# Kernel tuning notes

Hardware: AMD Instinct MI355X
Metric: run time of the kernel (lower is better)

Reference implementation:

```python
import jax, jax.numpy as jnp
import numpy as np

N_NODES = 50000
N_EDGES = 1600000
NUM_REL = 3
HID = 64
IN_DIM = 3
EDGE_DIM = 6
DEC_H = 32
Q1, Q2 = 5000.0, 10000.0


def _glorot(key, shape):
    fan_in, fan_out = shape[-2], shape[-1]
    lim = float(np.sqrt(6.0 / (fan_in + fan_out)))
    return jax.random.uniform(key, shape, jnp.float32, -lim, lim)


def setup_inputs() -> dict:
    key = jax.random.key(0)
    ks = jax.random.split(key, 20)
    x = jax.random.normal(ks[0], (N_NODES, IN_DIM), jnp.float32)
    edge_index = jax.random.randint(ks[1], (2, N_EDGES), 0, N_NODES, jnp.int64)
    edge_attr = jax.random.uniform(ks[2], (N_EDGES, EDGE_DIM), jnp.float32)
    # first column is distance in km; spread over [0, 15000) to hit all 3 bins
    edge_attr = edge_attr.at[:, 0].set(edge_attr[:, 0] * 15000.0)
    inp = {"x": x, "edge_index": edge_index, "edge_attr": edge_attr}
    dims = [IN_DIM, HID, HID]
    for i, din in enumerate(dims):
        inp[f"w{i}"] = _glorot(ks[3 + 3 * i], (NUM_REL, din, HID))
        inp[f"root{i}"] = _glorot(ks[4 + 3 * i], (din, HID))
        inp[f"b{i}"] = jnp.zeros((HID,), jnp.float32)
    dec_in = 2 * HID + EDGE_DIM
    inp["dw1"] = _glorot(ks[13], (dec_in, DEC_H))
    inp["db1"] = jnp.zeros((DEC_H,), jnp.float32)
    inp["dw2"] = _glorot(ks[14], (DEC_H, DEC_H // 2))
    inp["db2"] = jnp.zeros((DEC_H // 2,), jnp.float32)
    inp["dw3"] = _glorot(ks[15], (DEC_H // 2, 1))
    inp["db3"] = jnp.zeros((1,), jnp.float32)
    return inp


def _rgcn_conv(x, src, dst, edge_type, W, root, b):
    # PyG RGCNConv: per-relation mean aggregation of neighbor features,
    # then transform; plus root weight and bias.
    n = x.shape[0]
    xj = x[src]  # [E, in] gather
    out = x @ root + b
    for r in range(NUM_REL):
        m = (edge_type == r).astype(x.dtype)[:, None]  # [E,1]
        s = jax.ops.segment_sum(xj * m, dst, num_segments=n)   # [N,in]
        c = jax.ops.segment_sum(m, dst, num_segments=n)        # [N,1]
        h = s / jnp.maximum(c, 1.0)
        out = out + h @ W[r]
    return out


def reference(x, edge_index, edge_attr,
              w0, root0, b0, w1, root1, b1, w2, root2, b2,
              dw1, db1, dw2, db2, dw3, db3):
    dist = edge_attr[:, 0]
    edge_type = (dist > Q1).astype(jnp.int32) + (dist > Q2).astype(jnp.int32)
    src, dst = edge_index[0], edge_index[1]
    h = x
    for W, root, b in ((w0, root0, b0), (w1, root1, b1), (w2, root2, b2)):
        h = jax.nn.relu(_rgcn_conv(h, src, dst, edge_type, W, root, b))
        # dropout is identity in eval mode
    dec_in = jnp.concatenate([h[src], h[dst], edge_attr], axis=-1)  # [E, 134]
    z = jax.nn.relu(dec_in @ dw1 + db1)
    z = jax.nn.relu(z @ dw2 + db2)
    return (z @ dw3 + db3).squeeze(-1)
```

## Files before the change

kernel.cpp:

```cpp
#include <hip/hip_runtime.h>
#include <stdint.h>

#define N_NODES 50000
#define N_EDGES 1600000
#define NBLK_N 196
#define NB 391
#define BPAD 8192
#define CHUNK 4096
#define NWG_PREP 391

__device__ inline float bf2f(uint16_t u) {
  union { uint32_t i; float f; } c; c.i = (uint32_t)u << 16; return c.f;
}
__device__ inline uint16_t f2bf(float f) {
  union { uint32_t i; float f; } c; c.f = f;
  uint32_t b = c.i;
  b += 0x7FFFu + ((b >> 16) & 1u);
  return (uint16_t)(b >> 16);
}

__device__ inline uint32_t enc8(float v) {
  union { float f; uint32_t i; } c; c.f = v;
  uint32_t u = c.i;
  int t = (int)(((u + 0x80000u) >> 20) & 0x7FFu) - 960;
  t = t < 0 ? 0 : (t > 126 ? 126 : t);
  return ((u >> 24) & 0x80u) | (uint32_t)t;
}
__device__ inline float dec8(uint32_t b) {
  uint32_t m = b & 0x7Fu;
  union { uint32_t i; float f; } c;
  c.i = ((b & 0x80u) << 24) | ((m + 960u) << 20);
  return m ? c.f : 0.0f;
}

__global__ __launch_bounds__(256) void k_prep(const int* __restrict__ ei,
                                              const float* __restrict__ ea,
                                              int* __restrict__ bcur,
                                              uint32_t* __restrict__ pairbuf) {
  __shared__ int hist[NB];
  __shared__ int hbase[NB];
  int t = threadIdx.x;
  int base = blockIdx.x * CHUNK;
  for (int i = t; i < NB; i += 256) hist[i] = 0;
  __syncthreads();

  uint32_t wreg[16];
  int breg[16];
  #pragma unroll
  for (int k = 0; k < 16; k++) {
    int e = base + t + k * 256;
    breg[k] = -1;
    if (e < N_EDGES) {
      float dist = ea[(size_t)e * 6];
      int rel = (dist > 5000.0f) + (dist > 10000.0f);
      int s = ei[e];
      int d = ei[N_EDGES + e];
      wreg[k] = (uint32_t)s | ((uint32_t)rel << 16) | ((uint32_t)(d & 127) << 24);
      breg[k] = d >> 7;
      atomicAdd(&hist[breg[k]], 1);
    }
  }
  __syncthreads();
  for (int i = t; i < NB; i += 256) {
    int h = hist[i];
    hbase[i] = h ? atomicAdd(&bcur[i], h) : 0;
    hist[i] = 0;
  }
  __syncthreads();
  #pragma unroll
  for (int k = 0; k < 16; k++) {
    int b = breg[k];
    if (b >= 0) {
      int r = atomicAdd(&hist[b], 1);
      pairbuf[(size_t)b * BPAD + hbase[b] + r] = wreg[k];
    }
  }
}

__global__ __launch_bounds__(256) void k_count(const uint32_t* __restrict__ pairbuf,
                                               const int* __restrict__ bcur,
                                               int* __restrict__ cnt3) {
  __shared__ int lc[384];
  int b = blockIdx.x;
  int t = threadIdx.x;
  for (int i = t; i < 384; i += 256) lc[i] = 0;
  int cnt = bcur[b];
  __syncthreads();
  const uint32_t* pb = pairbuf + (size_t)b * BPAD;
  for (int i = t; i < cnt; i += 256) {
    uint32_t w = pb[i];
    int dl  = (int)(w >> 24);
    int rel = (int)((w >> 16) & 3u);
    atomicAdd(&lc[dl * 3 + rel], 1);
  }
  __syncthreads();
  int gbase = b * 384;
  for (int j = t; j < 384; j += 256) {
    int node = (b << 7) + (j / 3);
    if (node < N_NODES) cnt3[gbase + j] = lc[j];
  }
}

__global__ __launch_bounds__(256) void k_scanA(const int* __restrict__ cnt3,
                                               int* __restrict__ excl,
                                               int* __restrict__ bsum) {
  __shared__ int s[256];
  int t = threadIdx.x;
  int n = blockIdx.x * 256 + t;
  int deg = 0;
  if (n < N_NODES) deg = cnt3[3 * n] + cnt3[3 * n + 1] + cnt3[3 * n + 2];
  s[t] = deg;
  __syncthreads();
  for (int ofs = 1; ofs < 256; ofs <<= 1) {
    int v = (t >= ofs) ? s[t - ofs] : 0;
    __syncthreads();
    s[t] += v;
    __syncthreads();
  }
  if (n < N_NODES) excl[n] = s[t] - deg;
  if (t == 255) bsum[blockIdx.x] = s[255];
}

__global__ __launch_bounds__(256) void k_scanB(int* __restrict__ bsum) {
  __shared__ int s[256];
  int t = threadIdx.x;
  int v = (t < NBLK_N) ? bsum[t] : 0;
  s[t] = v;
  __syncthreads();
  for (int ofs = 1; ofs < 256; ofs <<= 1) {
    int u = (t >= ofs) ? s[t - ofs] : 0;
    __syncthreads();
    s[t] += u;
    __syncthreads();
  }
  if (t < NBLK_N) bsum[t] = s[t] - v;
}

__global__ __launch_bounds__(256) void k_scanC(const int* __restrict__ cnt3,
                                               const int* __restrict__ excl,
                                               const int* __restrict__ bsum,
                                               int4* __restrict__ meta,
                                               const float* __restrict__ x,
                                               float4* __restrict__ x4) {
  int n = blockIdx.x * 256 + threadIdx.x;
  if (n >= N_NODES) return;
  meta[n] = make_int4(bsum[blockIdx.x] + excl[n],
                      cnt3[3 * n], cnt3[3 * n + 1], cnt3[3 * n + 2]);
  x4[n] = make_float4(x[n * 3], x[n * 3 + 1], x[n * 3 + 2], 0.0f);
}

__global__ __launch_bounds__(256) void k_scat2(const uint32_t* __restrict__ pairbuf,
                                               const int* __restrict__ bcur,
                                               const int4* __restrict__ meta,
                                               uint32_t* __restrict__ csr) {
  __shared__ int lcur[128];
  int b = blockIdx.x;
  int t = threadIdx.x;
  int node0 = b << 7;
  if (t < 128) {
    int n = node0 + t;
    lcur[t] = (n < N_NODES) ? meta[n].x : 0;
  }
  int cnt = bcur[b];
  __syncthreads();
  const uint32_t* pb = pairbuf + (size_t)b * BPAD;
  for (int i = t; i < cnt; i += 256) {
    uint32_t w = pb[i];
    int dl = (int)(w >> 24);
    int p = atomicAdd(&lcur[dl], 1);
    csr[p] = w & 0x00FFFFFFu;
  }
}

__global__ __launch_bounds__(256) void k_layer0(const float4* __restrict__ x4,
                                                const float* __restrict__ W0,
                                                const float* __restrict__ root0,
                                                const float* __restrict__ b0,
                                                const int4* __restrict__ meta,
                                                const uint32_t* __restrict__ csr,
                                                float* __restrict__ hout,
                                                uint16_t* __restrict__ hbf) {
  __shared__ float sW[576], sR[192], sb[64];
  int t = threadIdx.x;
  for (int i = t; i < 576; i += 256) sW[i] = W0[i];
  for (int i = t; i < 192; i += 256) sR[i] = root0[i];
  if (t < 64) sb[t] = b0[t];
  __syncthreads();
  int wid = t >> 6, lane = t & 63;
  int n = blockIdx.x * 4 + wid;
  int4 md = meta[n];
  int off = md.x, c0 = md.y, c1 = md.z, c2 = md.w;
  int cnt = c0 + c1 + c2;
  float a00 = 0, a01 = 0, a02 = 0, a10 = 0, a11 = 0, a12 = 0, a20 = 0, a21 = 0, a22 = 0;
  for (int base = 0; base < cnt; base += 64) {
    int idx = base + lane;
    float4 v = make_float4(0, 0, 0, 0);
    int r = 3;
    if (idx < cnt) {
      uint32_t u = csr[off + idx];
      r = (int)(u >> 16);
      v = x4[u & 0xFFFFu];
    }
    a00 += (r == 0) ? v.x : 0.0f; a01 += (r == 0) ? v.y : 0.0f; a02 += (r == 0) ? v.z : 0.0f;
    a10 += (r == 1) ? v.x : 0.0f; a11 += (r == 1) ? v.y : 0.0f; a12 += (r == 1) ? v.z : 0.0f;
    a20 += (r == 2) ? v.x : 0.0f; a21 += (r == 2) ? v.y : 0.0f; a22 += (r == 2) ? v.z : 0.0f;
  }
  #pragma unroll
  for (int d = 1; d < 64; d <<= 1) {
    a00 += __shfl_xor(a00, d); a01 += __shfl_xor(a01, d); a02 += __shfl_xor(a02, d);
    a10 += __shfl_xor(a10, d); a11 += __shfl_xor(a11, d); a12 += __shfl_xor(a12, d);
    a20 += __shfl_xor(a20, d); a21 += __shfl_xor(a21, d); a22 += __shfl_xor(a22, d);
  }
  float i0 = 1.0f / (float)(c0 > 1 ? c0 : 1);
  float i1 = 1.0f / (float)(c1 > 1 ? c1 : 1);
  float i2 = 1.0f / (float)(c2 > 1 ? c2 : 1);
  float4 xn = x4[n];
  float in[12];
  in[0] = xn.x; in[1] = xn.y; in[2] = xn.z;
  in[3] = a00 * i0; in[4] = a01 * i0; in[5] = a02 * i0;
  in[6] = a10 * i1; in[7] = a11 * i1; in[8] = a12 * i1;
  in[9] = a20 * i2; in[10] = a21 * i2; in[11] = a22 * i2;
  float acc = sb[lane];
  #pragma unroll
  for (int k = 0; k < 3; k++) acc = fmaf(in[k], sR[k * 64 + lane], acc);
  #pragma unroll
  for (int k = 0; k < 9; k++) acc = fmaf(in[3 + k], sW[k * 64 + lane], acc);
  float h = fmaxf(acc, 0.0f);
  hout[(size_t)n * 64 + lane] = h;
  hbf[(size_t)n * 64 + lane] = f2bf(h);
}

#define ACC(E, V) { int r_ = (int)((E) >> 16); \
  a0 += (r_ == 0) ? (V) : 0.0f; a1 += (r_ == 1) ? (V) : 0.0f; a2 += (r_ == 2) ? (V) : 0.0f; }

__global__ __launch_bounds__(256) void k_agg(const uint16_t* __restrict__ hbf,
                                             const int4* __restrict__ meta,
                                             const uint32_t* __restrict__ csr,
                                             float* __restrict__ mbuf) {
  int t = threadIdx.x, wid = t >> 6, lane = t & 63;
  int n = blockIdx.x * 4 + wid;
  int4 md = meta[n];
  int off = __builtin_amdgcn_readfirstlane(md.x);
  int c0  = __builtin_amdgcn_readfirstlane(md.y);
  int c1  = __builtin_amdgcn_readfirstlane(md.z);
  int c2  = __builtin_amdgcn_readfirstlane(md.w);
  int cnt = c0 + c1 + c2;
  const uint32_t* cp = csr + off;
  float a0 = 0, a1 = 0, a2 = 0;
  int i = 0;
  for (; i + 8 <= cnt; i += 8) {
    uint32_t e0 = cp[i],     e1 = cp[i + 1], e2 = cp[i + 2], e3 = cp[i + 3];
    uint32_t e4 = cp[i + 4], e5 = cp[i + 5], e6 = cp[i + 6], e7 = cp[i + 7];
    float v0 = bf2f(hbf[(int)((e0 & 0xFFFFu) << 6) + lane]);
    float v1 = bf2f(hbf[(int)((e1 & 0xFFFFu) << 6) + lane]);
    float v2 = bf2f(hbf[(int)((e2 & 0xFFFFu) << 6) + lane]);
    float v3 = bf2f(hbf[(int)((e3 & 0xFFFFu) << 6) + lane]);
    float v4 = bf2f(hbf[(int)((e4 & 0xFFFFu) << 6) + lane]);
    float v5 = bf2f(hbf[(int)((e5 & 0xFFFFu) << 6) + lane]);
    float v6 = bf2f(hbf[(int)((e6 & 0xFFFFu) << 6) + lane]);
    float v7 = bf2f(hbf[(int)((e7 & 0xFFFFu) << 6) + lane]);
    ACC(e0, v0) ACC(e1, v1) ACC(e2, v2) ACC(e3, v3)
    ACC(e4, v4) ACC(e5, v5) ACC(e6, v6) ACC(e7, v7)
  }
  for (; i < cnt; i++) {
    uint32_t e = cp[i];
    float v = bf2f(hbf[(int)((e & 0xFFFFu) << 6) + lane]);
    ACC(e, v)
  }
  float* mb = mbuf + (size_t)n * 192;
  mb[lane]       = a0 * (1.0f / (float)(c0 > 1 ? c0 : 1));
  mb[64 + lane]  = a1 * (1.0f / (float)(c1 > 1 ? c1 : 1));
  mb[128 + lane] = a2 * (1.0f / (float)(c2 > 1 ? c2 : 1));
}

__global__ __launch_bounds__(256) void k_gemm(const float* __restrict__ hin,
                                              const float* __restrict__ mbuf,
                                              const float* __restrict__ W,
                                              const float* __restrict__ root,
                                              const float* __restrict__ b,
                                              float* __restrict__ hout,
                                              uint16_t* __restrict__ hbf) {
  __shared__ float As[64 * 84];
  __shared__ float Bs[64 * 64];
  __shared__ float sb[64];
  int t = threadIdx.x;
  int bn = blockIdx.x * 64;
  if (t < 64) sb[t] = b[t];
  int tn = t & 15, to = t >> 4;
  float acc[4][4] = {};
  for (int kb = 0; kb < 4; kb++) {
    const float4* Bsrc = (const float4*)((kb == 0) ? root : (W + (size_t)(kb - 1) * 4096));
    for (int i2 = t; i2 < 1024; i2 += 256) ((float4*)Bs)[i2] = Bsrc[i2];
    int r = t >> 2;
    int node = bn + r;
    bool ok = node < N_NODES;
    const float* Arow = (kb == 0) ? (hin + (size_t)node * 64)
                                  : (mbuf + (size_t)node * 192 + (size_t)(kb - 1) * 64);
    #pragma unroll
    for (int ii = 0; ii < 4; ii++) {
      int c4 = (t & 3) + 4 * ii;
      float4 v = ok ? ((const float4*)Arow)[c4] : make_float4(0, 0, 0, 0);
      *(float4*)&As[r * 84 + c4 * 4] = v;
    }
    __syncthreads();
    #pragma unroll
    for (int k4 = 0; k4 < 16; k4++) {
      float4 a0 = *(const float4*)&As[(tn)      * 84 + k4 * 4];
      float4 a1 = *(const float4*)&As[(tn + 16) * 84 + k4 * 4];
      float4 a2 = *(const float4*)&As[(tn + 32) * 84 + k4 * 4];
      float4 a3 = *(const float4*)&As[(tn + 48) * 84 + k4 * 4];
      float4 b0 = *(const float4*)&Bs[(k4 * 4 + 0) * 64 + to * 4];
      float4 b1 = *(const float4*)&Bs[(k4 * 4 + 1) * 64 + to * 4];
      float4 b2 = *(const float4*)&Bs[(k4 * 4 + 2) * 64 + to * 4];
      float4 b3 = *(const float4*)&Bs[(k4 * 4 + 3) * 64 + to * 4];
      const float* av[4] = {&a0.x, &a1.x, &a2.x, &a3.x};
      const float* bv[4] = {&b0.x, &b1.x, &b2.x, &b3.x};
      #pragma unroll
      for (int c = 0; c < 4; c++)
        #pragma unroll
        for (int i3 = 0; i3 < 4; i3++)
          #pragma unroll
          for (int j = 0; j < 4; j++)
            acc[i3][j] = fmaf(av[i3][c], bv[c][j], acc[i3][j]);
    }
    __syncthreads();
  }
  #pragma unroll
  for (int i3 = 0; i3 < 4; i3++) {
    int node = bn + tn + 16 * i3;
    if (node < N_NODES) {
      float4 o;
      o.x = fmaxf(acc[i3][0] + sb[to * 4 + 0], 0.0f);
      o.y = fmaxf(acc[i3][1] + sb[to * 4 + 1], 0.0f);
      o.z = fmaxf(acc[i3][2] + sb[to * 4 + 2], 0.0f);
      o.w = fmaxf(acc[i3][3] + sb[to * 4 + 3], 0.0f);
      *(float4*)(hout + (size_t)node * 64 + to * 4) = o;
      if (hbf) {
        uint2 pk;
        pk.x = (uint32_t)f2bf(o.x) | ((uint32_t)f2bf(o.y) << 16);
        pk.y = (uint32_t)f2bf(o.z) | ((uint32_t)f2bf(o.w) << 16);
        *(uint2*)(hbf + (size_t)node * 64 + to * 4) = pk;
      }
    }
  }
}

__global__ __launch_bounds__(256) void k_pq2(const float* __restrict__ h,
                                             const float* __restrict__ dw1,
                                             const float* __restrict__ db1,
                                             uint8_t* __restrict__ Pb,
                                             uint8_t* __restrict__ Qb) {
  __shared__ float As[64 * 84];
  __shared__ float Bs[64 * 64];
  __shared__ float sdb1[32];
  int t = threadIdx.x;
  int bn = blockIdx.x * 64;
  if (t < 32) sdb1[t] = db1[t];
  {
    int r = t >> 2;
    int node = bn + r;
    bool ok = node < N_NODES;
    const float* Arow = h + (size_t)node * 64;
    #pragma unroll
    for (int ii = 0; ii < 4; ii++) {
      int c4 = (t & 3) + 4 * ii;
      float4 v = ok ? ((const float4*)Arow)[c4] : make_float4(0, 0, 0, 0);
      *(float4*)&As[r * 84 + c4 * 4] = v;
    }
  }
  for (int i = t; i < 4096; i += 256) {
    int k = i >> 6, j = i & 63;
    Bs[i] = (j < 32) ? dw1[k * 32 + j] : dw1[(64 + k) * 32 + (j - 32)];
  }
  __syncthreads();
  int tn = t & 15, to = t >> 4;
  float acc[4][4] = {};
  #pragma unroll
  for (int k4 = 0; k4 < 16; k4++) {
    float4 a0 = *(const float4*)&As[(tn)      * 84 + k4 * 4];
    float4 a1 = *(const float4*)&As[(tn + 16) * 84 + k4 * 4];
    float4 a2 = *(const float4*)&As[(tn + 32) * 84 + k4 * 4];
    float4 a3 = *(const float4*)&As[(tn + 48) * 84 + k4 * 4];
    float4 b0 = *(const float4*)&Bs[(k4 * 4 + 0) * 64 + to * 4];
    float4 b1 = *(const float4*)&Bs[(k4 * 4 + 1) * 64 + to * 4];
    float4 b2 = *(const float4*)&Bs[(k4 * 4 + 2) * 64 + to * 4];
    float4 b3 = *(const float4*)&Bs[(k4 * 4 + 3) * 64 + to * 4];
    const float* av[4] = {&a0.x, &a1.x, &a2.x, &a3.x};
    const float* bv[4] = {&b0.x, &b1.x, &b2.x, &b3.x};
    #pragma unroll
    for (int c = 0; c < 4; c++)
      #pragma unroll
      for (int i3 = 0; i3 < 4; i3++)
        #pragma unroll
        for (int j = 0; j < 4; j++)
          acc[i3][j] = fmaf(av[i3][c], bv[c][j], acc[i3][j]);
  }
  bool isP = (to < 8);
  float bias0 = isP ? sdb1[to * 4 + 0] : 0.0f;
  float bias1 = isP ? sdb1[to * 4 + 1] : 0.0f;
  float bias2 = isP ? sdb1[to * 4 + 2] : 0.0f;
  float bias3 = isP ? sdb1[to * 4 + 3] : 0.0f;
  #pragma unroll
  for (int i3 = 0; i3 < 4; i3++) {
    int node = bn + tn + 16 * i3;
    if (node < N_NODES) {
      uint32_t pk = enc8(acc[i3][0] + bias0)
                  | (enc8(acc[i3][1] + bias1) << 8)
                  | (enc8(acc[i3][2] + bias2) << 16)
                  | (enc8(acc[i3][3] + bias3) << 24);
      if (isP) *(uint32_t*)(Pb + (size_t)node * 32 + to * 4) = pk;
      else     *(uint32_t*)(Qb + (size_t)node * 32 + (to - 8) * 4) = pk;
    }
  }
}

__global__ __launch_bounds__(256) void k_dec(const int* __restrict__ ei,
                                             const float* __restrict__ ea,
                                             const uint8_t* __restrict__ Pb,
                                             const uint8_t* __restrict__ Qb,
                                             const float* __restrict__ dw1,
                                             const float* __restrict__ dw2,
                                             const float* __restrict__ db2,
                                             const float* __restrict__ dw3,
                                             const float* __restrict__ db3,
                                             float* __restrict__ out) {
  __shared__ float C[6 * 32], W2[32 * 16], sb2[16], W3[16];
  __shared__ float sb3;
  int t = threadIdx.x;
  for (int i = t; i < 192; i += 256) C[i] = dw1[128 * 32 + i];
  for (int i = t; i < 512; i += 256) W2[i] = dw2[i];
  if (t < 16) { sb2[t] = db2[t]; W3[t] = dw3[t]; }
  if (t == 0) sb3 = db3[0];
  __syncthreads();
  int e = blockIdx.x * 256 + t;
  int s = ei[e];
  int d = ei[N_EDGES + e];
  float ea6[6];
  #pragma unroll
  for (int i = 0; i < 6; i++) ea6[i] = ea[(size_t)e * 6 + i];
  uint4 pv0 = *(const uint4*)(Pb + (size_t)s * 32);
  uint4 pv1 = *(const uint4*)(Pb + (size_t)s * 32 + 16);
  uint4 qv0 = *(const uint4*)(Qb + (size_t)d * 32);
  uint4 qv1 = *(const uint4*)(Qb + (size_t)d * 32 + 16);
  uint32_t pw[8] = {pv0.x, pv0.y, pv0.z, pv0.w, pv1.x, pv1.y, pv1.z, pv1.w};
  uint32_t qw[8] = {qv0.x, qv0.y, qv0.z, qv0.w, qv1.x, qv1.y, qv1.z, qv1.w};
  float z1[32];
  #pragma unroll
  for (int w = 0; w < 8; w++) {
    #pragma unroll
    for (int c = 0; c < 4; c++) {
      int j = w * 4 + c;
      float v = dec8((pw[w] >> (8 * c)) & 0xFFu) + dec8((qw[w] >> (8 * c)) & 0xFFu);
      #pragma unroll
      for (int k = 0; k < 6; k++) v = fmaf(ea6[k], C[k * 32 + j], v);
      z1[j] = fmaxf(v, 0.0f);
    }
  }
  float o = sb3;
  #pragma unroll
  for (int i = 0; i < 16; i++) {
    float z = sb2[i];
    #pragma unroll
    for (int j = 0; j < 32; j++) z = fmaf(z1[j], W2[j * 16 + i], z);
    o = fmaf(fmaxf(z, 0.0f), W3[i], o);
  }
  out[e] = o;
}

extern "C" void kernel_launch(void* const* d_in, const int* in_sizes, int n_in,
                              void* d_out, int out_size, void* d_ws, size_t ws_size,
                              hipStream_t stream) {
  const float* x      = (const float*)d_in[0];
  const int*   ei     = (const int*)d_in[1];
  const float* ea     = (const float*)d_in[2];
  const float* w0     = (const float*)d_in[3];
  const float* root0  = (const float*)d_in[4];
  const float* b0     = (const float*)d_in[5];
  const float* w1     = (const float*)d_in[6];
  const float* root1  = (const float*)d_in[7];
  const float* b1     = (const float*)d_in[8];
  const float* w2     = (const float*)d_in[9];
  const float* root2  = (const float*)d_in[10];
  const float* b2     = (const float*)d_in[11];
  const float* dw1    = (const float*)d_in[12];
  const float* db1    = (const float*)d_in[13];
  const float* dw2    = (const float*)d_in[14];
  const float* db2    = (const float*)d_in[15];
  const float* dw3    = (const float*)d_in[16];
  const float* db3    = (const float*)d_in[17];
  float* out = (float*)d_out;

  char* w = (char*)d_ws;
  int* cnt3        = (int*)w;       w += (size_t)N_NODES * 3 * 4;
  int* bcur        = (int*)w;       w += (size_t)NB * 4;
  int4* meta       = (int4*)w;      w += (size_t)N_NODES * 16;
  uint32_t* csr    = (uint32_t*)w;  w += (size_t)N_EDGES * 4;
  float4* x4       = (float4*)w;    w += (size_t)N_NODES * 16;
  float* h1        = (float*)w;     w += (size_t)N_NODES * 64 * 4;
  float* h2        = (float*)w;     w += (size_t)N_NODES * 64 * 4;
  float* mbuf      = (float*)w;     w += (size_t)N_NODES * 192 * 4;
  uint16_t* hbf1   = (uint16_t*)w;  w += (size_t)N_NODES * 64 * 2;
  uint16_t* hbf2   = (uint16_t*)w;  w += (size_t)N_NODES * 64 * 2;
  uint8_t* Pb      = (uint8_t*)hbf1;
  uint8_t* Qb      = (uint8_t*)hbf2;
  uint32_t* pairbuf = (uint32_t*)h1;
  int* excl        = (int*)mbuf;
  int* bsum        = (int*)mbuf + N_NODES;

  hipMemsetAsync(bcur, 0, (size_t)NB * 4, stream);

  k_prep   <<<NWG_PREP, 256, 0, stream>>>(ei, ea, bcur, pairbuf);
  k_count  <<<NB, 256, 0, stream>>>(pairbuf, bcur, cnt3);
  k_scanA  <<<NBLK_N, 256, 0, stream>>>(cnt3, excl, bsum);
  k_scanB  <<<1, 256, 0, stream>>>(bsum);
  k_scanC  <<<NBLK_N, 256, 0, stream>>>(cnt3, excl, bsum, meta, x, x4);
  k_scat2  <<<NB, 256, 0, stream>>>(pairbuf, bcur, meta, csr);

  k_layer0 <<<N_NODES / 4, 256, 0, stream>>>(x4, w0, root0, b0, meta, csr, h1, hbf1);

  k_agg    <<<N_NODES / 4, 256, 0, stream>>>(hbf1, meta, csr, mbuf);
  k_gemm   <<<(N_NODES + 63) / 64, 256, 0, stream>>>(h1, mbuf, w1, root1, b1, h2, hbf2);

  k_agg    <<<N_NODES / 4, 256, 0, stream>>>(hbf2, meta, csr, mbuf);
  k_gemm   <<<(N_NODES + 63) / 64, 256, 0, stream>>>(h2, mbuf, w2, root2, b2, h1, (uint16_t*)nullptr);

  k_pq2    <<<(N_NODES + 63) / 64, 256, 0, stream>>>(h1, dw1, db1, Pb, Qb);
  k_dec    <<<N_EDGES / 256, 256, 0, stream>>>(ei, ea, Pb, Qb, dw1, dw2, db2, dw3, db3, out);
}
```

Before: 350.5 us.

## Store gathered node features in hardware FP8 and vectorize decoder weight reads

Hidden features gathered by the aggregation kernels are now stored as 8-bit FP8 instead of bf16, halving the bytes pulled per neighbour gather. The custom software 8-bit encode and decode in the P/Q and decoder path is replaced by hardware FP8 pack and convert instructions. The decoder also transposes W2 in shared memory so it can be read with float4 loads. FP8 E4M3 keeps fewer mantissa bits than bf16, so the mean aggregation loses precision, and values are clamped at 440.

```diff
diff --git a/kernel.cpp b/kernel.cpp
--- a/kernel.cpp
+++ b/kernel.cpp
@@ -9,28 +9,20 @@
 #define CHUNK 4096
 #define NWG_PREP 391
 
+typedef float fvec2 __attribute__((ext_vector_type(2)));
+
 __device__ inline float bf2f(uint16_t u) {
   union { uint32_t i; float f; } c; c.i = (uint32_t)u << 16; return c.f;
 }
-__device__ inline uint16_t f2bf(float f) {
-  union { uint32_t i; float f; } c; c.f = f;
-  uint32_t b = c.i;
-  b += 0x7FFFu + ((b >> 16) & 1u);
-  return (uint16_t)(b >> 16);
-}
-
-__device__ inline uint32_t enc8(float v) {
-  union { float f; uint32_t i; } c; c.f = v;
-  uint32_t u = c.i;
-  int t = (int)(((u + 0x80000u) >> 20) & 0x7FFu) - 960;
-  t = t < 0 ? 0 : (t > 126 ? 126 : t);
-  return ((u >> 24) & 0x80u) | (uint32_t)t;
-}
-__device__ inline float dec8(uint32_t b) {
-  uint32_t m = b & 0x7Fu;
-  union { uint32_t i; float f; } c;
-  c.i = ((b & 0x80u) << 24) | ((m + 960u) << 20);
-  return m ? c.f : 0.0f;
+
+__device__ inline uint32_t pk4_fp8(float a, float b, float c, float d) {
+  a = fminf(fmaxf(a, -440.0f), 440.0f);
+  b = fminf(fmaxf(b, -440.0f), 440.0f);
+  c = fminf(fmaxf(c, -440.0f), 440.0f);
+  d = fminf(fmaxf(d, -440.0f), 440.0f);
+  int pk = __builtin_amdgcn_cvt_pk_fp8_f32(a, b, 0, false);
+  pk = __builtin_amdgcn_cvt_pk_fp8_f32(c, d, pk, true);
+  return (uint32_t)pk;
 }
 
 __global__ __launch_bounds__(256) void k_prep(const int* __restrict__ ei,
@@ -179,7 +171,7 @@
                                                 const int4* __restrict__ meta,
                                                 const uint32_t* __restrict__ csr,
                                                 float* __restrict__ hout,
-                                                uint16_t* __restrict__ hbf) {
+                                                uint8_t* __restrict__ hf8) {
   __shared__ float sW[576], sR[192], sb[64];
   int t = threadIdx.x;
   for (int i = t; i < 576; i += 256) sW[i] = W0[i];
@@ -227,13 +219,15 @@
   for (int k = 0; k < 9; k++) acc = fmaf(in[3 + k], sW[k * 64 + lane], acc);
   float h = fmaxf(acc, 0.0f);
   hout[(size_t)n * 64 + lane] = h;
-  hbf[(size_t)n * 64 + lane] = f2bf(h);
+  float hc = fminf(h, 440.0f);
+  int p8 = __builtin_amdgcn_cvt_pk_fp8_f32(hc, hc, 0, false);
+  hf8[(size_t)n * 64 + lane] = (uint8_t)(p8 & 0xFF);
 }
 
 #define ACC(E, V) { int r_ = (int)((E) >> 16); \
   a0 += (r_ == 0) ? (V) : 0.0f; a1 += (r_ == 1) ? (V) : 0.0f; a2 += (r_ == 2) ? (V) : 0.0f; }
 
-__global__ __launch_bounds__(256) void k_agg(const uint16_t* __restrict__ hbf,
+__global__ __launch_bounds__(256) void k_agg(const uint8_t* __restrict__ hf8,
                                              const int4* __restrict__ meta,
                                              const uint32_t* __restrict__ csr,
                                              float* __restrict__ mbuf) {
@@ -251,20 +245,29 @@
   for (; i + 8 <= cnt; i += 8) {
     uint32_t e0 = cp[i],     e1 = cp[i + 1], e2 = cp[i + 2], e3 = cp[i + 3];
     uint32_t e4 = cp[i + 4], e5 = cp[i + 5], e6 = cp[i + 6], e7 = cp[i + 7];
-    float v0 = bf2f(hbf[(int)((e0 & 0xFFFFu) << 6) + lane]);
-    float v1 = bf2f(hbf[(int)((e1 & 0xFFFFu) << 6) + lane]);
-    float v2 = bf2f(hbf[(int)((e2 & 0xFFFFu) << 6) + lane]);
-    float v3 = bf2f(hbf[(int)((e3 & 0xFFFFu) << 6) + lane]);
-    float v4 = bf2f(hbf[(int)((e4 & 0xFFFFu) << 6) + lane]);
-    float v5 = bf2f(hbf[(int)((e5 & 0xFFFFu) << 6) + lane]);
-    float v6 = bf2f(hbf[(int)((e6 & 0xFFFFu) << 6) + lane]);
-    float v7 = bf2f(hbf[(int)((e7 & 0xFFFFu) << 6) + lane]);
+    int b0 = hf8[(int)((e0 & 0xFFFFu) << 6) + lane];
+    int b1 = hf8[(int)((e1 & 0xFFFFu) << 6) + lane];
+    int b2 = hf8[(int)((e2 & 0xFFFFu) << 6) + lane];
+    int b3 = hf8[(int)((e3 & 0xFFFFu) << 6) + lane];
+    int b4 = hf8[(int)((e4 & 0xFFFFu) << 6) + lane];
+    int b5 = hf8[(int)((e5 & 0xFFFFu) << 6) + lane];
+    int b6 = hf8[(int)((e6 & 0xFFFFu) << 6) + lane];
+    int b7 = hf8[(int)((e7 & 0xFFFFu) << 6) + lane];
+    float v0 = __builtin_amdgcn_cvt_f32_fp8(b0, 0);
+    float v1 = __builtin_amdgcn_cvt_f32_fp8(b1, 0);
+    float v2 = __builtin_amdgcn_cvt_f32_fp8(b2, 0);
+    float v3 = __builtin_amdgcn_cvt_f32_fp8(b3, 0);
+    float v4 = __builtin_amdgcn_cvt_f32_fp8(b4, 0);
+    float v5 = __builtin_amdgcn_cvt_f32_fp8(b5, 0);
+    float v6 = __builtin_amdgcn_cvt_f32_fp8(b6, 0);
+    float v7 = __builtin_amdgcn_cvt_f32_fp8(b7, 0);
     ACC(e0, v0) ACC(e1, v1) ACC(e2, v2) ACC(e3, v3)
     ACC(e4, v4) ACC(e5, v5) ACC(e6, v6) ACC(e7, v7)
   }
   for (; i < cnt; i++) {
     uint32_t e = cp[i];
-    float v = bf2f(hbf[(int)((e & 0xFFFFu) << 6) + lane]);
+    int b = hf8[(int)((e & 0xFFFFu) << 6) + lane];
+    float v = __builtin_amdgcn_cvt_f32_fp8(b, 0);
     ACC(e, v)
   }
   float* mb = mbuf + (size_t)n * 192;
@@ -279,7 +282,7 @@
                                               const float* __restrict__ root,
                                               const float* __restrict__ b,
                                               float* __restrict__ hout,
-                                              uint16_t* __restrict__ hbf) {
+                                              uint8_t* __restrict__ hf8) {
   __shared__ float As[64 * 84];
   __shared__ float Bs[64 * 64];
   __shared__ float sb[64];
@@ -335,11 +338,9 @@
       o.z = fmaxf(acc[i3][2] + sb[to * 4 + 2], 0.0f);
       o.w = fmaxf(acc[i3][3] + sb[to * 4 + 3], 0.0f);
       *(float4*)(hout + (size_t)node * 64 + to * 4) = o;
-      if (hbf) {
-        uint2 pk;
-        pk.x = (uint32_t)f2bf(o.x) | ((uint32_t)f2bf(o.y) << 16);
-        pk.y = (uint32_t)f2bf(o.z) | ((uint32_t)f2bf(o.w) << 16);
-        *(uint2*)(hbf + (size_t)node * 64 + to * 4) = pk;
+      if (hf8) {
+        uint32_t pk = pk4_fp8(o.x, o.y, o.z, o.w);
+        *(uint32_t*)(hf8 + (size_t)node * 64 + to * 4) = pk;
       }
     }
   }
@@ -404,10 +405,8 @@
   for (int i3 = 0; i3 < 4; i3++) {
     int node = bn + tn + 16 * i3;
     if (node < N_NODES) {
-      uint32_t pk = enc8(acc[i3][0] + bias0)
-                  | (enc8(acc[i3][1] + bias1) << 8)
-                  | (enc8(acc[i3][2] + bias2) << 16)
-                  | (enc8(acc[i3][3] + bias3) << 24);
+      uint32_t pk = pk4_fp8(acc[i3][0] + bias0, acc[i3][1] + bias1,
+                            acc[i3][2] + bias2, acc[i3][3] + bias3);
       if (isP) *(uint32_t*)(Pb + (size_t)node * 32 + to * 4) = pk;
       else     *(uint32_t*)(Qb + (size_t)node * 32 + (to - 8) * 4) = pk;
     }
@@ -424,11 +423,14 @@
                                              const float* __restrict__ dw3,
                                              const float* __restrict__ db3,
                                              float* __restrict__ out) {
-  __shared__ float C[6 * 32], W2[32 * 16], sb2[16], W3[16];
+  __shared__ float C[6 * 32], W2T[16 * 32], sb2[16], W3[16];
   __shared__ float sb3;
   int t = threadIdx.x;
   for (int i = t; i < 192; i += 256) C[i] = dw1[128 * 32 + i];
-  for (int i = t; i < 512; i += 256) W2[i] = dw2[i];
+  for (int i = t; i < 512; i += 256) {
+    int r = i >> 5, c = i & 31;
+    W2T[i] = dw2[c * 16 + r];
+  }
   if (t < 16) { sb2[t] = db2[t]; W3[t] = dw3[t]; }
   if (t == 0) sb3 = db3[0];
   __syncthreads();
@@ -447,21 +449,39 @@
   float z1[32];
   #pragma unroll
   for (int w = 0; w < 8; w++) {
+    fvec2 pl = __builtin_amdgcn_cvt_pk_f32_fp8((int)pw[w], false);
+    fvec2 ph = __builtin_amdgcn_cvt_pk_f32_fp8((int)pw[w], true);
+    fvec2 ql = __builtin_amdgcn_cvt_pk_f32_fp8((int)qw[w], false);
+    fvec2 qh = __builtin_amdgcn_cvt_pk_f32_fp8((int)qw[w], true);
+    float v0 = pl.x + ql.x;
+    float v1 = pl.y + ql.y;
+    float v2 = ph.x + qh.x;
+    float v3 = ph.y + qh.y;
     #pragma unroll
-    for (int c = 0; c < 4; c++) {
-      int j = w * 4 + c;
-      float v = dec8((pw[w] >> (8 * c)) & 0xFFu) + dec8((qw[w] >> (8 * c)) & 0xFFu);
-      #pragma unroll
-      for (int k = 0; k < 6; k++) v = fmaf(ea6[k], C[k * 32 + j], v);
-      z1[j] = fmaxf(v, 0.0f);
-    }
+    for (int k = 0; k < 6; k++) {
+      float4 cv = *(const float4*)&C[k * 32 + w * 4];
+      v0 = fmaf(ea6[k], cv.x, v0);
+      v1 = fmaf(ea6[k], cv.y, v1);
+      v2 = fmaf(ea6[k], cv.z, v2);
+      v3 = fmaf(ea6[k], cv.w, v3);
+    }
+    z1[w * 4 + 0] = fmaxf(v0, 0.0f);
+    z1[w * 4 + 1] = fmaxf(v1, 0.0f);
+    z1[w * 4 + 2] = fmaxf(v2, 0.0f);
+    z1[w * 4 + 3] = fmaxf(v3, 0.0f);
   }
   float o = sb3;
   #pragma unroll
   for (int i = 0; i < 16; i++) {
     float z = sb2[i];
     #pragma unroll
-    for (int j = 0; j < 32; j++) z = fmaf(z1[j], W2[j * 16 + i], z);
+    for (int j4 = 0; j4 < 8; j4++) {
+      float4 wv = *(const float4*)&W2T[i * 32 + j4 * 4];
+      z = fmaf(z1[j4 * 4 + 0], wv.x, z);
+      z = fmaf(z1[j4 * 4 + 1], wv.y, z);
+      z = fmaf(z1[j4 * 4 + 2], wv.z, z);
+      z = fmaf(z1[j4 * 4 + 3], wv.w, z);
+    }
     o = fmaf(fmaxf(z, 0.0f), W3[i], o);
   }
   out[e] = o;
@@ -499,10 +519,12 @@
   float* h1        = (float*)w;     w += (size_t)N_NODES * 64 * 4;
   float* h2        = (float*)w;     w += (size_t)N_NODES * 64 * 4;
   float* mbuf      = (float*)w;     w += (size_t)N_NODES * 192 * 4;
-  uint16_t* hbf1   = (uint16_t*)w;  w += (size_t)N_NODES * 64 * 2;
-  uint16_t* hbf2   = (uint16_t*)w;  w += (size_t)N_NODES * 64 * 2;
-  uint8_t* Pb      = (uint8_t*)hbf1;
-  uint8_t* Qb      = (uint8_t*)hbf2;
+  uint8_t* slot1   = (uint8_t*)w;   w += (size_t)N_NODES * 64;
+  uint8_t* slot2   = (uint8_t*)w;   w += (size_t)N_NODES * 64;
+  uint8_t* hf8_1   = slot1;
+  uint8_t* hf8_2   = slot2;
+  uint8_t* Pb      = slot1;
+  uint8_t* Qb      = slot2;
   uint32_t* pairbuf = (uint32_t*)h1;
   int* excl        = (int*)mbuf;
   int* bsum        = (int*)mbuf + N_NODES;
@@ -516,13 +538,13 @@
   k_scanC  <<<NBLK_N, 256, 0, stream>>>(cnt3, excl, bsum, meta, x, x4);
   k_scat2  <<<NB, 256, 0, stream>>>(pairbuf, bcur, meta, csr);
 
-  k_layer0 <<<N_NODES / 4, 256, 0, stream>>>(x4, w0, root0, b0, meta, csr, h1, hbf1);
-
-  k_agg    <<<N_NODES / 4, 256, 0, stream>>>(hbf1, meta, csr, mbuf);
-  k_gemm   <<<(N_NODES + 63) / 64, 256, 0, stream>>>(h1, mbuf, w1, root1, b1, h2, hbf2);
-
-  k_agg    <<<N_NODES / 4, 256, 0, stream>>>(hbf2, meta, csr, mbuf);
-  k_gemm   <<<(N_NODES + 63) / 64, 256, 0, stream>>>(h2, mbuf, w2, root2, b2, h1, (uint16_t*)nullptr);
+  k_layer0 <<<N_NODES / 4, 256, 0, stream>>>(x4, w0, root0, b0, meta, csr, h1, hf8_1);
+
+  k_agg    <<<N_NODES / 4, 256, 0, stream>>>(hf8_1, meta, csr, mbuf);
+  k_gemm   <<<(N_NODES + 63) / 64, 256, 0, stream>>>(h1, mbuf, w1, root1, b1, h2, hf8_2);
+
+  k_agg    <<<N_NODES / 4, 256, 0, stream>>>(hf8_2, meta, csr, mbuf);
+  k_gemm   <<<(N_NODES + 63) / 64, 256, 0, stream>>>(h2, mbuf, w2, root2, b2, h1, (uint8_t*)nullptr);
 
   k_pq2    <<<(N_NODES + 63) / 64, 256, 0, stream>>>(h1, dw1, db1, Pb, Qb);
   k_dec    <<<N_EDGES / 256, 256, 0, stream>>>(ei, ea, Pb, Qb, dw1, dw2, db2, dw3, db3, out);
```

Measured after the change: 333.1 us. -5.0%, faster.
